# Kernel optimization log

Hardware: AMD Instinct MI355X
Metric: run time of the kernel (lower is better)

Reference implementation:

```python
import jax, jax.numpy as jnp
import numpy as np


def setup_inputs() -> dict:
    key = jax.random.key(0)
    ks = jax.random.split(key, 5)
    B, S, D, H, E = 2, 2048, 1024, 2816, 8
    x = jax.random.normal(ks[0], (B, S, D), dtype=jnp.float32)
    Wg = jax.random.normal(ks[1], (E, D), dtype=jnp.float32) * 0.02
    W1 = jax.random.normal(ks[2], (E, H, D), dtype=jnp.float32) * 0.02
    W2 = jax.random.normal(ks[3], (E, H, D), dtype=jnp.float32) * 0.02
    W3 = jax.random.normal(ks[4], (E, D, H), dtype=jnp.float32) * 0.02
    return {"x": x, "Wg": Wg, "W1": W1, "W2": W2, "W3": W3}


TOP_K = 2


def reference(x, Wg, W1, W2, W3):
    B, S, D = x.shape
    E = Wg.shape[0]
    xt = x.reshape(B * S, D)  # [T, D]
    # gating: raw logits, NO softmax (matches original module)
    scores = xt @ Wg.T  # [T, E]
    topk_scores, topk_idx = jax.lax.top_k(scores, TOP_K)  # [T, K]
    # dense per-expert SwiGLU FFN over all tokens, combined with sparse weights
    gate = jax.nn.silu(jnp.einsum('td,ehd->teh', xt, W1))  # [T, E, H]
    up = jnp.einsum('td,ehd->teh', xt, W2)                 # [T, E, H]
    y = jnp.einsum('teh,edh->ted', gate * up, W3)           # [T, E, D]
    # combine weights: w[t, e] = sum_k topk_scores[t, k] * (topk_idx[t, k] == e)
    onehot = jax.nn.one_hot(topk_idx, E, dtype=x.dtype)     # [T, K, E]
    w = jnp.einsum('tke,tk->te', onehot, topk_scores)       # [T, E]
    out = jnp.einsum('te,ted->td', w, y)                    # [T, D]
    return out.reshape(B, S, D)
```

## Files before the change

### kernel.cpp

```cpp
#include <hip/hip_runtime.h>
#include <hip/hip_bf16.h>


#define T_TOK 4096
#define DDIM 1024
#define HDIM 2816
#define NEXP 8

typedef __attribute__((ext_vector_type(8))) short short8;
typedef __attribute__((ext_vector_type(4))) short short4v;
typedef __attribute__((ext_vector_type(4))) float floatx4;

__device__ __forceinline__ short f2bf(float f) {
  union { float f; unsigned int u; } v; v.f = f;
  unsigned int u = v.u;
  u += 0x7FFFu + ((u >> 16) & 1u);
  return (short)(u >> 16);
}

__global__ __launch_bounds__(256) void zero_kernel(float4* __restrict__ out4, int* __restrict__ counts) {
  int i = blockIdx.x * 256 + threadIdx.x;
  out4[i] = make_float4(0.f, 0.f, 0.f, 0.f);
  if (blockIdx.x == 0 && threadIdx.x < NEXP) counts[threadIdx.x] = 0;
}

__global__ __launch_bounds__(64) void gating_kernel(const float* __restrict__ x,
    const float* __restrict__ Wg, short* __restrict__ xbf,
    int* __restrict__ counts, int* __restrict__ tlist, float* __restrict__ wlist) {
  int t = blockIdx.x;
  int lane = threadIdx.x;
  const float* xt = x + (size_t)t * DDIM;
  float xr[16];
#pragma unroll
  for (int j = 0; j < 16; ++j) xr[j] = xt[j * 64 + lane];
  short* xbt = xbf + (size_t)t * DDIM;
#pragma unroll
  for (int j = 0; j < 16; ++j) xbt[j * 64 + lane] = f2bf(xr[j]);
  float s[NEXP];
#pragma unroll
  for (int e = 0; e < NEXP; ++e) {
    const float* wge = Wg + e * DDIM;
    float p = 0.f;
#pragma unroll
    for (int j = 0; j < 16; ++j) p += xr[j] * wge[j * 64 + lane];
#pragma unroll
    for (int o = 32; o > 0; o >>= 1) p += __shfl_xor(p, o, 64);
    s[e] = p;
  }
  if (lane == 0) {
    int e1 = 0; float s1 = s[0];
#pragma unroll
    for (int e = 1; e < NEXP; ++e) if (s[e] > s1) { s1 = s[e]; e1 = e; }
    int e2 = -1; float s2 = -1e30f;
#pragma unroll
    for (int e = 0; e < NEXP; ++e) if (e != e1 && s[e] > s2) { s2 = s[e]; e2 = e; }
    int slot = atomicAdd(&counts[e1], 1);
    tlist[e1 * T_TOK + slot] = t; wlist[e1 * T_TOK + slot] = s1;
    slot = atomicAdd(&counts[e2], 1);
    tlist[e2 * T_TOK + slot] = t; wlist[e2 * T_TOK + slot] = s2;
  }
}

__global__ void offsets_kernel(const int* __restrict__ counts, int* __restrict__ offs) {
  if (threadIdx.x == 0 && blockIdx.x == 0) {
    int run = 0;
    for (int e = 0; e < NEXP; ++e) { offs[e] = run; run += counts[e]; }
  }
}

__global__ __launch_bounds__(256) void ffn1_kernel(const short* __restrict__ xbf,
    const float* __restrict__ W1, const float* __restrict__ W2,
    const int* __restrict__ counts, const int* __restrict__ offs,
    const int* __restrict__ tlist, short* __restrict__ hmat) {
  int e = blockIdx.z;
  int cnt = counts[e];
  int m0 = blockIdx.y * 128;
  if (m0 >= cnt) return;
  int n0 = blockIdx.x * 64;
  __shared__ __attribute__((aligned(16))) short As[128 * 40];
  __shared__ __attribute__((aligned(16))) short Bs1[64 * 40];
  __shared__ __attribute__((aligned(16))) short Bs2[64 * 40];
  __shared__ int toks[128];
  int tid = threadIdx.x;
  if (tid < 128) {
    int m = m0 + tid;
    toks[tid] = tlist[e * T_TOK + (m < cnt ? m : cnt - 1)];
  }
  __syncthreads();
  const float* W1e = W1 + (size_t)e * HDIM * DDIM + (size_t)n0 * DDIM;
  const float* W2e = W2 + (size_t)e * HDIM * DDIM + (size_t)n0 * DDIM;
  int lane = tid & 63, wid = tid >> 6;
  int wr = wid >> 1, wc = wid & 1;
  int lrow = lane & 15, lq = lane >> 4;
  floatx4 accg[4][2], accu[4][2];
#pragma unroll
  for (int i = 0; i < 4; ++i)
#pragma unroll
    for (int j = 0; j < 2; ++j) {
      accg[i][j] = (floatx4){0.f, 0.f, 0.f, 0.f};
      accu[i][j] = (floatx4){0.f, 0.f, 0.f, 0.f};
    }
  int ar0 = tid >> 2, ac0 = (tid & 3) * 8;
  int br0 = tid >> 3, bc0 = (tid & 7) * 4;
  int tokA0 = toks[ar0], tokA1 = toks[ar0 + 64];
  const short* xA0 = xbf + (size_t)tokA0 * DDIM + ac0;
  const short* xA1 = xbf + (size_t)tokA1 * DDIM + ac0;
  const float* pB1a = W1e + (size_t)br0 * DDIM + bc0;
  const float* pB1b = W1e + (size_t)(br0 + 32) * DDIM + bc0;
  const float* pB2a = W2e + (size_t)br0 * DDIM + bc0;
  const float* pB2b = W2e + (size_t)(br0 + 32) * DDIM + bc0;

  for (int kk = 0; kk < DDIM; kk += 32) {
    *(short8*)&As[ar0 * 40 + ac0]        = *(const short8*)(xA0 + kk);
    *(short8*)&As[(ar0 + 64) * 40 + ac0] = *(const short8*)(xA1 + kk);
    {
      float4 v1a = *(const float4*)(pB1a + kk);
      float4 v1b = *(const float4*)(pB1b + kk);
      float4 v2a = *(const float4*)(pB2a + kk);
      float4 v2b = *(const float4*)(pB2b + kk);
      *(short4v*)&Bs1[br0 * 40 + bc0]        = (short4v){f2bf(v1a.x), f2bf(v1a.y), f2bf(v1a.z), f2bf(v1a.w)};
      *(short4v*)&Bs1[(br0 + 32) * 40 + bc0] = (short4v){f2bf(v1b.x), f2bf(v1b.y), f2bf(v1b.z), f2bf(v1b.w)};
      *(short4v*)&Bs2[br0 * 40 + bc0]        = (short4v){f2bf(v2a.x), f2bf(v2a.y), f2bf(v2a.z), f2bf(v2a.w)};
      *(short4v*)&Bs2[(br0 + 32) * 40 + bc0] = (short4v){f2bf(v2b.x), f2bf(v2b.y), f2bf(v2b.z), f2bf(v2b.w)};
    }
    __syncthreads();
    short8 a[4], b1[2], b2[2];
#pragma unroll
    for (int mf = 0; mf < 4; ++mf)
      a[mf] = *(short8*)&As[(wr * 64 + mf * 16 + lrow) * 40 + lq * 8];
#pragma unroll
    for (int nf = 0; nf < 2; ++nf) {
      b1[nf] = *(short8*)&Bs1[(wc * 32 + nf * 16 + lrow) * 40 + lq * 8];
      b2[nf] = *(short8*)&Bs2[(wc * 32 + nf * 16 + lrow) * 40 + lq * 8];
    }
#pragma unroll
    for (int mf = 0; mf < 4; ++mf)
#pragma unroll
      for (int nf = 0; nf < 2; ++nf) {
        accg[mf][nf] = __builtin_amdgcn_mfma_f32_16x16x32_bf16(a[mf], b1[nf], accg[mf][nf], 0, 0, 0);
        accu[mf][nf] = __builtin_amdgcn_mfma_f32_16x16x32_bf16(a[mf], b2[nf], accu[mf][nf], 0, 0, 0);
      }
    __syncthreads();
  }
  int base = offs[e];
#pragma unroll
  for (int mf = 0; mf < 4; ++mf)
#pragma unroll
    for (int r = 0; r < 4; ++r) {
      int mloc = wr * 64 + mf * 16 + lq * 4 + r;
      if (m0 + mloc < cnt) {
        size_t row = (size_t)(base + m0 + mloc);
#pragma unroll
        for (int nf = 0; nf < 2; ++nf) {
          float g = accg[mf][nf][r];
          float u = accu[mf][nf][r];
          float h = g / (1.f + __expf(-g)) * u;
          hmat[row * HDIM + n0 + wc * 32 + nf * 16 + lrow] = f2bf(h);
        }
      }
    }
}

__global__ __launch_bounds__(256) void ffn2_kernel(const short* __restrict__ hmat,
    const float* __restrict__ W3,
    const int* __restrict__ counts, const int* __restrict__ offs,
    const int* __restrict__ tlist, const float* __restrict__ wlist,
    float* __restrict__ out) {
  int e = blockIdx.z;
  int cnt = counts[e];
  int m0 = blockIdx.y * 128;
  if (m0 >= cnt) return;
  int n0 = blockIdx.x * 128;
  __shared__ __attribute__((aligned(16))) short As[128 * 40];
  __shared__ __attribute__((aligned(16))) short Bs[128 * 40];
  __shared__ int toks[128];
  __shared__ float wts[128];
  int tid = threadIdx.x;
  if (tid < 128) {
    int m = m0 + tid;
    int mc = m < cnt ? m : cnt - 1;
    toks[tid] = tlist[e * T_TOK + mc];
    wts[tid] = (m < cnt) ? wlist[e * T_TOK + m] : 0.f;
  }
  __syncthreads();
  int base = offs[e];
  const float* W3e = W3 + (size_t)e * DDIM * HDIM + (size_t)n0 * HDIM;
  int lane = tid & 63, wid = tid >> 6;
  int wr = wid >> 1, wc = wid & 1;
  int lrow = lane & 15, lq = lane >> 4;
  floatx4 acc[4][4];
#pragma unroll
  for (int i = 0; i < 4; ++i)
#pragma unroll
    for (int j = 0; j < 4; ++j) acc[i][j] = (floatx4){0.f, 0.f, 0.f, 0.f};
  int ar0 = tid >> 2, ac0 = (tid & 3) * 8;
  int br0 = tid >> 3, bc0 = (tid & 7) * 4;
  int mA0 = m0 + ar0;       mA0 = mA0 < cnt ? mA0 : cnt - 1;
  int mA1 = m0 + ar0 + 64;  mA1 = mA1 < cnt ? mA1 : cnt - 1;
  const short* hA0 = hmat + (size_t)(base + mA0) * HDIM + ac0;
  const short* hA1 = hmat + (size_t)(base + mA1) * HDIM + ac0;

  for (int kk = 0; kk < HDIM; kk += 32) {
    *(short8*)&As[ar0 * 40 + ac0]        = *(const short8*)(hA0 + kk);
    *(short8*)&As[(ar0 + 64) * 40 + ac0] = *(const short8*)(hA1 + kk);
#pragma unroll
    for (int l = 0; l < 4; ++l) {
      int r = br0 + l * 32;
      float4 v = *(const float4*)(W3e + (size_t)r * HDIM + kk + bc0);
      *(short4v*)&Bs[r * 40 + bc0] = (short4v){f2bf(v.x), f2bf(v.y), f2bf(v.z), f2bf(v.w)};
    }
    __syncthreads();
    short8 a[4], b[4];
#pragma unroll
    for (int mf = 0; mf < 4; ++mf)
      a[mf] = *(short8*)&As[(wr * 64 + mf * 16 + lrow) * 40 + lq * 8];
#pragma unroll
    for (int nf = 0; nf < 4; ++nf)
      b[nf] = *(short8*)&Bs[(wc * 64 + nf * 16 + lrow) * 40 + lq * 8];
#pragma unroll
    for (int mf = 0; mf < 4; ++mf)
#pragma unroll
      for (int nf = 0; nf < 4; ++nf)
        acc[mf][nf] = __builtin_amdgcn_mfma_f32_16x16x32_bf16(a[mf], b[nf], acc[mf][nf], 0, 0, 0);
    __syncthreads();
  }
#pragma unroll
  for (int mf = 0; mf < 4; ++mf)
#pragma unroll
    for (int r = 0; r < 4; ++r) {
      int mloc = wr * 64 + mf * 16 + lq * 4 + r;
      if (m0 + mloc < cnt) {
        int t = toks[mloc];
        float w = wts[mloc];
        float* orow = out + (size_t)t * DDIM + n0 + wc * 64 + lrow;
#pragma unroll
        for (int nf = 0; nf < 4; ++nf)
          atomicAdd(orow + nf * 16, w * acc[mf][nf][r]);
      }
    }
}

extern "C" void kernel_launch(void* const* d_in, const int* in_sizes, int n_in,
                              void* d_out, int out_size, void* d_ws, size_t ws_size,
                              hipStream_t stream) {
  const float* x  = (const float*)d_in[0];
  const float* Wg = (const float*)d_in[1];
  const float* W1 = (const float*)d_in[2];
  const float* W2 = (const float*)d_in[3];
  const float* W3 = (const float*)d_in[4];
  float* out = (float*)d_out;
  char* ws = (char*)d_ws;
  int*   counts = (int*)(ws + 0);
  int*   offs   = (int*)(ws + 256);
  int*   tlist  = (int*)(ws + 512);
  float* wlist  = (float*)(ws + 512 + 131072);
  short* xbf    = (short*)(ws + 512 + 2 * 131072);
  short* hmat   = (short*)(ws + 8651264);

  zero_kernel<<<4096, 256, 0, stream>>>((float4*)out, counts);
  gating_kernel<<<4096, 64, 0, stream>>>(x, Wg, xbf, counts, tlist, wlist);
  offsets_kernel<<<1, 64, 0, stream>>>(counts, offs);
  ffn1_kernel<<<dim3(HDIM / 64, T_TOK / 128, NEXP), 256, 0, stream>>>(xbf, W1, W2, counts, offs, tlist, hmat);
  ffn2_kernel<<<dim3(DDIM / 128, T_TOK / 128, NEXP), 256, 0, stream>>>(hmat, W3, counts, offs, tlist, wlist, out);
}
```

Baseline: 653.6 us.

## Pre-convert expert weights to bf16 and use direct global-to-LDS loads with deterministic combine

When the workspace is large enough, the expert weights are first converted to bf16 in a separate pass. New FFN kernels then stream the bf16 operands straight into LDS with global_load_lds, replacing per-tile fp32 loads and conversions. FFN2 writes per-expert rows to a partial buffer, and a combine kernel blends the two expert outputs per token, replacing the float atomics into the output. The cost is a full weight conversion on every call plus extra workspace traffic, and the main loops are single-buffered with no padding against LDS bank conflicts.

```diff
diff --git a/kernel.cpp b/kernel.cpp
--- a/kernel.cpp
+++ b/kernel.cpp
@@ -1,5 +1,6 @@
 #include <hip/hip_runtime.h>
 #include <hip/hip_bf16.h>
+#include <stdint.h>
 
 
 #define T_TOK 4096
@@ -17,6 +18,249 @@
   u += 0x7FFFu + ((u >> 16) & 1u);
   return (short)(u >> 16);
 }
+
+__device__ __forceinline__ void gl2lds16(const void* g, void* l) {
+  __builtin_amdgcn_global_load_lds(
+      (const __attribute__((address_space(1))) void*)g,
+      (__attribute__((address_space(3))) void*)l, 16, 0, 0);
+}
+
+
+__global__ void offsets_kernel(const int* __restrict__ counts, int* __restrict__ offs) {
+  if (threadIdx.x == 0 && blockIdx.x == 0) {
+    int run = 0;
+    for (int e = 0; e < NEXP; ++e) { offs[e] = run; run += counts[e]; }
+  }
+}
+
+
+__global__ __launch_bounds__(64) void zero_counts_kernel(int* __restrict__ counts) {
+  if (threadIdx.x < NEXP) counts[threadIdx.x] = 0;
+}
+
+__global__ __launch_bounds__(256) void convert_kernel(
+    const float* __restrict__ W1, const float* __restrict__ W2, const float* __restrict__ W3,
+    short* __restrict__ W1bf, short* __restrict__ W2bf, short* __restrict__ W3bf) {
+  int z = blockIdx.y;
+  const float* src = (z == 0) ? W1 : (z == 1) ? W2 : W3;
+  short* dst = (z == 0) ? W1bf : (z == 1) ? W2bf : W3bf;
+  size_t i = ((size_t)blockIdx.x * 256 + threadIdx.x) * 8;
+  float4 v0 = *(const float4*)(src + i);
+  float4 v1 = *(const float4*)(src + i + 4);
+  short8 s = {f2bf(v0.x), f2bf(v0.y), f2bf(v0.z), f2bf(v0.w),
+              f2bf(v1.x), f2bf(v1.y), f2bf(v1.z), f2bf(v1.w)};
+  *(short8*)(dst + i) = s;
+}
+
+__global__ __launch_bounds__(64) void gating_fast_kernel(const float* __restrict__ x,
+    const float* __restrict__ Wg, short* __restrict__ xbf,
+    int* __restrict__ counts, int* __restrict__ tlist,
+    int* __restrict__ re, int* __restrict__ rs, float* __restrict__ rw) {
+  int t = blockIdx.x;
+  int lane = threadIdx.x;
+  const float* xt = x + (size_t)t * DDIM;
+  float xr[16];
+#pragma unroll
+  for (int j = 0; j < 16; ++j) xr[j] = xt[j * 64 + lane];
+  short* xbt = xbf + (size_t)t * DDIM;
+#pragma unroll
+  for (int j = 0; j < 16; ++j) xbt[j * 64 + lane] = f2bf(xr[j]);
+  float s[NEXP];
+#pragma unroll
+  for (int e = 0; e < NEXP; ++e) {
+    const float* wge = Wg + e * DDIM;
+    float p = 0.f;
+#pragma unroll
+    for (int j = 0; j < 16; ++j) p += xr[j] * wge[j * 64 + lane];
+#pragma unroll
+    for (int o = 32; o > 0; o >>= 1) p += __shfl_xor(p, o, 64);
+    s[e] = p;
+  }
+  if (lane == 0) {
+    int e1 = 0; float s1 = s[0];
+#pragma unroll
+    for (int e = 1; e < NEXP; ++e) if (s[e] > s1) { s1 = s[e]; e1 = e; }
+    int e2 = -1; float s2 = -1e30f;
+#pragma unroll
+    for (int e = 0; e < NEXP; ++e) if (e != e1 && s[e] > s2) { s2 = s[e]; e2 = e; }
+    int slot = atomicAdd(&counts[e1], 1);
+    tlist[e1 * T_TOK + slot] = t;
+    re[2 * t] = e1; rs[2 * t] = slot; rw[2 * t] = s1;
+    slot = atomicAdd(&counts[e2], 1);
+    tlist[e2 * T_TOK + slot] = t;
+    re[2 * t + 1] = e2; rs[2 * t + 1] = slot; rw[2 * t + 1] = s2;
+  }
+}
+
+__global__ __launch_bounds__(256) void ffn1_fast_kernel(const short* __restrict__ xbf,
+    const short* __restrict__ W1bf, const short* __restrict__ W2bf,
+    const int* __restrict__ counts, const int* __restrict__ offs,
+    const int* __restrict__ tlist, short* __restrict__ hmat) {
+  int e = blockIdx.z;
+  int cnt = counts[e];
+  int m0 = blockIdx.y * 128;
+  if (m0 >= cnt) return;
+  int n0 = blockIdx.x * 64;
+  __shared__ __attribute__((aligned(16))) short As[128 * 32];
+  __shared__ __attribute__((aligned(16))) short Bs1[64 * 32];
+  __shared__ __attribute__((aligned(16))) short Bs2[64 * 32];
+  __shared__ int toks[128];
+  int tid = threadIdx.x;
+  if (tid < 128) {
+    int m = m0 + tid;
+    toks[tid] = tlist[e * T_TOK + (m < cnt ? m : cnt - 1)];
+  }
+  __syncthreads();
+  int lane = tid & 63, w = tid >> 6;
+  int wr = w >> 1, wc = w & 1;
+  int lrow = lane & 15, lq = lane >> 4;
+  int lr = lane >> 2;
+  int lc = (lane & 3) * 8;
+  const short* pA0 = xbf + (size_t)toks[w * 32 + lr] * DDIM + lc;
+  const short* pA1 = xbf + (size_t)toks[w * 32 + 16 + lr] * DDIM + lc;
+  const short* b1e = W1bf + (size_t)e * HDIM * DDIM;
+  const short* b2e = W2bf + (size_t)e * HDIM * DDIM;
+  const short* pB1 = b1e + (size_t)(n0 + w * 16 + lr) * DDIM + lc;
+  const short* pB2 = b2e + (size_t)(n0 + w * 16 + lr) * DDIM + lc;
+  void* lA0 = (void*)&As[(2 * w) * 512];
+  void* lA1 = (void*)&As[(2 * w + 1) * 512];
+  void* lB1 = (void*)&Bs1[w * 512];
+  void* lB2 = (void*)&Bs2[w * 512];
+  floatx4 accg[4][2], accu[4][2];
+#pragma unroll
+  for (int i = 0; i < 4; ++i)
+#pragma unroll
+    for (int j = 0; j < 2; ++j) {
+      accg[i][j] = (floatx4){0.f, 0.f, 0.f, 0.f};
+      accu[i][j] = (floatx4){0.f, 0.f, 0.f, 0.f};
+    }
+  for (int kk = 0; kk < DDIM; kk += 32) {
+    gl2lds16(pA0, lA0);
+    gl2lds16(pA1, lA1);
+    gl2lds16(pB1, lB1);
+    gl2lds16(pB2, lB2);
+    pA0 += 32; pA1 += 32; pB1 += 32; pB2 += 32;
+    __syncthreads();
+    short8 a[4], b1[2], b2[2];
+#pragma unroll
+    for (int mf = 0; mf < 4; ++mf)
+      a[mf] = *(short8*)&As[(wr * 64 + mf * 16 + lrow) * 32 + lq * 8];
+#pragma unroll
+    for (int nf = 0; nf < 2; ++nf) {
+      b1[nf] = *(short8*)&Bs1[(wc * 32 + nf * 16 + lrow) * 32 + lq * 8];
+      b2[nf] = *(short8*)&Bs2[(wc * 32 + nf * 16 + lrow) * 32 + lq * 8];
+    }
+#pragma unroll
+    for (int mf = 0; mf < 4; ++mf)
+#pragma unroll
+      for (int nf = 0; nf < 2; ++nf) {
+        accg[mf][nf] = __builtin_amdgcn_mfma_f32_16x16x32_bf16(a[mf], b1[nf], accg[mf][nf], 0, 0, 0);
+        accu[mf][nf] = __builtin_amdgcn_mfma_f32_16x16x32_bf16(a[mf], b2[nf], accu[mf][nf], 0, 0, 0);
+      }
+    __syncthreads();
+  }
+  int base = offs[e];
+#pragma unroll
+  for (int mf = 0; mf < 4; ++mf)
+#pragma unroll
+    for (int r = 0; r < 4; ++r) {
+      int mloc = wr * 64 + mf * 16 + lq * 4 + r;
+      if (m0 + mloc < cnt) {
+        size_t row = (size_t)(base + m0 + mloc);
+#pragma unroll
+        for (int nf = 0; nf < 2; ++nf) {
+          float g = accg[mf][nf][r];
+          float u = accu[mf][nf][r];
+          float h = g / (1.f + __expf(-g)) * u;
+          hmat[row * HDIM + n0 + wc * 32 + nf * 16 + lrow] = f2bf(h);
+        }
+      }
+    }
+}
+
+__global__ __launch_bounds__(256) void ffn2_fast_kernel(const short* __restrict__ hmat,
+    const short* __restrict__ W3bf,
+    const int* __restrict__ counts, const int* __restrict__ offs,
+    float* __restrict__ ypart) {
+  int e = blockIdx.z;
+  int cnt = counts[e];
+  int m0 = blockIdx.y * 128;
+  if (m0 >= cnt) return;
+  int n0 = blockIdx.x * 128;
+  int base = offs[e];
+  __shared__ __attribute__((aligned(16))) short As[128 * 32];
+  __shared__ __attribute__((aligned(16))) short Bs[128 * 32];
+  int tid = threadIdx.x;
+  int lane = tid & 63, w = tid >> 6;
+  int wr = w >> 1, wc = w & 1;
+  int lrow = lane & 15, lq = lane >> 4;
+  int lr = lane >> 2;
+  int lc = (lane & 3) * 8;
+  int gA0 = m0 + w * 32 + lr;      gA0 = gA0 < cnt ? gA0 : cnt - 1;
+  int gA1 = m0 + w * 32 + 16 + lr; gA1 = gA1 < cnt ? gA1 : cnt - 1;
+  const short* pA0 = hmat + (size_t)(base + gA0) * HDIM + lc;
+  const short* pA1 = hmat + (size_t)(base + gA1) * HDIM + lc;
+  const short* W3e = W3bf + (size_t)e * DDIM * HDIM;
+  const short* pB0 = W3e + (size_t)(n0 + w * 32 + lr) * HDIM + lc;
+  const short* pB1 = W3e + (size_t)(n0 + w * 32 + 16 + lr) * HDIM + lc;
+  void* lA0 = (void*)&As[(2 * w) * 512];
+  void* lA1 = (void*)&As[(2 * w + 1) * 512];
+  void* lB0 = (void*)&Bs[(2 * w) * 512];
+  void* lB1 = (void*)&Bs[(2 * w + 1) * 512];
+  floatx4 acc[4][4];
+#pragma unroll
+  for (int i = 0; i < 4; ++i)
+#pragma unroll
+    for (int j = 0; j < 4; ++j) acc[i][j] = (floatx4){0.f, 0.f, 0.f, 0.f};
+  for (int kk = 0; kk < HDIM; kk += 32) {
+    gl2lds16(pA0, lA0);
+    gl2lds16(pA1, lA1);
+    gl2lds16(pB0, lB0);
+    gl2lds16(pB1, lB1);
+    pA0 += 32; pA1 += 32; pB0 += 32; pB1 += 32;
+    __syncthreads();
+    short8 a[4], b[4];
+#pragma unroll
+    for (int mf = 0; mf < 4; ++mf)
+      a[mf] = *(short8*)&As[(wr * 64 + mf * 16 + lrow) * 32 + lq * 8];
+#pragma unroll
+    for (int nf = 0; nf < 4; ++nf)
+      b[nf] = *(short8*)&Bs[(wc * 64 + nf * 16 + lrow) * 32 + lq * 8];
+#pragma unroll
+    for (int mf = 0; mf < 4; ++mf)
+#pragma unroll
+      for (int nf = 0; nf < 4; ++nf)
+        acc[mf][nf] = __builtin_amdgcn_mfma_f32_16x16x32_bf16(a[mf], b[nf], acc[mf][nf], 0, 0, 0);
+    __syncthreads();
+  }
+#pragma unroll
+  for (int mf = 0; mf < 4; ++mf)
+#pragma unroll
+    for (int r = 0; r < 4; ++r) {
+      int mloc = wr * 64 + mf * 16 + lq * 4 + r;
+      if (m0 + mloc < cnt) {
+        float* orow = ypart + (size_t)(base + m0 + mloc) * DDIM + n0 + wc * 64 + lrow;
+#pragma unroll
+        for (int nf = 0; nf < 4; ++nf)
+          orow[nf * 16] = acc[mf][nf][r];
+      }
+    }
+}
+
+__global__ __launch_bounds__(256) void combine_kernel(const float4* __restrict__ ypart4,
+    const int* __restrict__ offs, const int* __restrict__ re, const int* __restrict__ rs,
+    const float* __restrict__ rw, float4* __restrict__ out4) {
+  int t = blockIdx.x;
+  int i = threadIdx.x;
+  int r0 = offs[re[2 * t]] + rs[2 * t];
+  int r1 = offs[re[2 * t + 1]] + rs[2 * t + 1];
+  float w0 = rw[2 * t], w1 = rw[2 * t + 1];
+  float4 a = ypart4[(size_t)r0 * 256 + i];
+  float4 b = ypart4[(size_t)r1 * 256 + i];
+  out4[(size_t)t * 256 + i] = make_float4(w0 * a.x + w1 * b.x, w0 * a.y + w1 * b.y,
+                                          w0 * a.z + w1 * b.z, w0 * a.w + w1 * b.w);
+}
+
 
 __global__ __launch_bounds__(256) void zero_kernel(float4* __restrict__ out4, int* __restrict__ counts) {
   int i = blockIdx.x * 256 + threadIdx.x;
@@ -58,13 +302,6 @@
     tlist[e1 * T_TOK + slot] = t; wlist[e1 * T_TOK + slot] = s1;
     slot = atomicAdd(&counts[e2], 1);
     tlist[e2 * T_TOK + slot] = t; wlist[e2 * T_TOK + slot] = s2;
-  }
-}
-
-__global__ void offsets_kernel(const int* __restrict__ counts, int* __restrict__ offs) {
-  if (threadIdx.x == 0 && blockIdx.x == 0) {
-    int run = 0;
-    for (int e = 0; e < NEXP; ++e) { offs[e] = run; run += counts[e]; }
   }
 }
 
@@ -240,6 +477,7 @@
     }
 }
 
+
 extern "C" void kernel_launch(void* const* d_in, const int* in_sizes, int n_in,
                               void* d_out, int out_size, void* d_ws, size_t ws_size,
                               hipStream_t stream) {
@@ -250,16 +488,43 @@
   const float* W3 = (const float*)d_in[4];
   float* out = (float*)d_out;
   char* ws = (char*)d_ws;
-  int*   counts = (int*)(ws + 0);
-  int*   offs   = (int*)(ws + 256);
-  int*   tlist  = (int*)(ws + 512);
-  float* wlist  = (float*)(ws + 512 + 131072);
-  short* xbf    = (short*)(ws + 512 + 2 * 131072);
-  short* hmat   = (short*)(ws + 8651264);
-
-  zero_kernel<<<4096, 256, 0, stream>>>((float4*)out, counts);
-  gating_kernel<<<4096, 64, 0, stream>>>(x, Wg, xbf, counts, tlist, wlist);
-  offsets_kernel<<<1, 64, 0, stream>>>(counts, offs);
-  ffn1_kernel<<<dim3(HDIM / 64, T_TOK / 128, NEXP), 256, 0, stream>>>(xbf, W1, W2, counts, offs, tlist, hmat);
-  ffn2_kernel<<<dim3(DDIM / 128, T_TOK / 128, NEXP), 256, 0, stream>>>(hmat, W3, counts, offs, tlist, wlist, out);
-}
+
+  const size_t NEED_FAST = 193167872ull;
+  if (ws_size >= NEED_FAST) {
+    int*   counts = (int*)(ws + 0);
+    int*   offs   = (int*)(ws + 256);
+    int*   tlist  = (int*)(ws + 512);
+    int*   re     = (int*)(ws + 131584);
+    int*   rs     = (int*)(ws + 164352);
+    float* rw     = (float*)(ws + 197120);
+    short* xbf    = (short*)(ws + 229888);
+    short* hmat   = (short*)(ws + 8618496);
+    short* W3bf   = (short*)(ws + 54755840);
+    short* W1bf   = (short*)(ws + 100893184);
+    short* W2bf   = (short*)(ws + 147030528);
+    float* ypart  = (float*)(ws + 100893184);
+
+    zero_counts_kernel<<<1, 64, 0, stream>>>(counts);
+    convert_kernel<<<dim3(11264, 3), 256, 0, stream>>>(W1, W2, W3, W1bf, W2bf, W3bf);
+    gating_fast_kernel<<<T_TOK, 64, 0, stream>>>(x, Wg, xbf, counts, tlist, re, rs, rw);
+    offsets_kernel<<<1, 64, 0, stream>>>(counts, offs);
+    ffn1_fast_kernel<<<dim3(HDIM / 64, T_TOK / 128, NEXP), 256, 0, stream>>>(
+        xbf, W1bf, W2bf, counts, offs, tlist, hmat);
+    ffn2_fast_kernel<<<dim3(DDIM / 128, T_TOK / 128, NEXP), 256, 0, stream>>>(
+        hmat, W3bf, counts, offs, ypart);
+    combine_kernel<<<T_TOK, 256, 0, stream>>>((const float4*)ypart, offs, re, rs, rw, (float4*)out);
+  } else {
+    int*   counts = (int*)(ws + 0);
+    int*   offs   = (int*)(ws + 256);
+    int*   tlist  = (int*)(ws + 512);
+    float* wlist  = (float*)(ws + 512 + 131072);
+    short* xbf    = (short*)(ws + 512 + 2 * 131072);
+    short* hmat   = (short*)(ws + 8651264);
+
+    zero_kernel<<<4096, 256, 0, stream>>>((float4*)out, counts);
+    gating_kernel<<<4096, 64, 0, stream>>>(x, Wg, xbf, counts, tlist, wlist);
+    offsets_kernel<<<1, 64, 0, stream>>>(counts, offs);
+    ffn1_kernel<<<dim3(HDIM / 64, T_TOK / 128, NEXP), 256, 0, stream>>>(xbf, W1, W2, counts, offs, tlist, hmat);
+    ffn2_kernel<<<dim3(DDIM / 128, T_TOK / 128, NEXP), 256, 0, stream>>>(hmat, W3, counts, offs, tlist, wlist, out);
+  }
+}
```

New measurement: 640.5 us. 2.0% less time.
